# Kernel optimization log

Hardware: AMD Instinct MI355X
Metric: run time of the kernel (lower is better)

## Reference

```python
import jax, jax.numpy as jnp
import numpy as np

# ---- constants matching init_kwargs ----
NUM_CLASSES = 20
NUM_GRID = 7
NUM_BBOX = 2
IN_SIZE = 448          # image_shapes = (448, 448)
IOU_THRESHOLD = 0.7    # self.num_threshold passed to batched_nms
SCORE_THRESHOLD = 0.1  # boxes[:, -1] > 0.1 reserve mask
M = NUM_GRID * NUM_GRID  # 49 boxes per image
BATCH = 16384


def setup_inputs() -> dict:
    key = jax.random.key(0)
    out_features = M * (NUM_CLASSES + 5 * NUM_BBOX)  # 1470
    x = jax.random.uniform(key, (BATCH, out_features), dtype=jnp.float32)
    return {"x": x}


def _iou_matrix(boxes):
    # boxes: [M, 4] in (x0, y0, x1, y1). Returns [M, M] pairwise IoU.
    area = jnp.clip(boxes[:, 2] - boxes[:, 0], 0) * jnp.clip(boxes[:, 3] - boxes[:, 1], 0)
    lt = jnp.maximum(boxes[:, None, :2], boxes[None, :, :2])   # [M, M, 2]
    rb = jnp.minimum(boxes[:, None, 2:], boxes[None, :, 2:])   # [M, M, 2]
    wh = jnp.clip(rb - lt, 0)
    inter = wh[..., 0] * wh[..., 1]
    union = area[:, None] + area[None, :] - inter
    return inter / jnp.maximum(union, 1e-9)


def _nms_keep(boxes, scores, labels, valid):
    # Per-image class-aware NMS (torchvision batched_nms semantics via coordinate offsets).
    # boxes [M,4], scores [M], labels [M] int, valid [M] bool -> keep mask [M] bool.
    max_coord = jnp.max(boxes)
    offs = labels.astype(boxes.dtype) * (max_coord + 1.0)
    b = boxes + offs[:, None]
    s = jnp.where(valid, scores, -jnp.inf)
    order = jnp.argsort(-s)                 # descending by score, invalid last
    bs = b[order]
    vs = valid[order]
    iou = _iou_matrix(bs)                   # [M, M]
    idx = jnp.arange(M)

    def step(suppressed, i):
        keep_i = vs[i] & ~suppressed[i]
        suppressed = suppressed | (keep_i & (iou[i] > IOU_THRESHOLD) & (idx > i))
        return suppressed, keep_i

    _, keep_sorted = jax.lax.scan(step, jnp.zeros((M,), bool), idx)
    return jnp.zeros((M,), bool).at[order].set(keep_sorted)


def reference(x):
    N = x.shape[0]
    x = x.reshape(N, M, NUM_CLASSES + 5 * NUM_BBOX)
    class_logits = x[..., :NUM_CLASSES]                       # [N, M, C]
    bb = x[..., NUM_CLASSES:].reshape(N, M, NUM_BBOX, 5)      # [N, M, B, 5]
    # pick the bbox with max confidence per cell
    best = jnp.argmax(bb[..., 4], axis=-1)                    # [N, M]
    yolo_bboxes = jnp.take_along_axis(bb, best[..., None, None], axis=2)[:, :, 0, :]  # [N, M, 5]

    probs = jax.nn.softmax(class_logits, axis=-1)
    labels = jnp.argmax(probs, axis=-1)                       # [N, M]

    # boxes_decode: grid offsets (x tiles, y repeats) then cx/cy/w/h -> corners
    g = jnp.arange(NUM_GRID, dtype=x.dtype)
    x_grid = jnp.tile(g, NUM_GRID)                            # [M]
    y_grid = jnp.repeat(g, NUM_GRID)                          # [M]
    cx = (yolo_bboxes[..., 0] + x_grid) / NUM_GRID
    cy = (yolo_bboxes[..., 1] + y_grid) / NUM_GRID
    hw = yolo_bboxes[..., 2] / 2
    hh = yolo_bboxes[..., 3] / 2
    W = jnp.asarray(IN_SIZE, x.dtype)
    H = jnp.asarray(IN_SIZE, x.dtype)
    x0 = (cx - hw) * W
    y0 = (cy - hh) * H
    x1 = (cx + hw) * W
    y1 = (cy + hh) * H
    scores = yolo_bboxes[..., 4]
    reserve_mask = scores > SCORE_THRESHOLD                   # [N, M]

    # clip_boxes_to_image
    x0 = jnp.clip(x0, 0, IN_SIZE); x1 = jnp.clip(x1, 0, IN_SIZE)
    y0 = jnp.clip(y0, 0, IN_SIZE); y1 = jnp.clip(y1, 0, IN_SIZE)
    boxes = jnp.stack([x0, y0, x1, y1], axis=-1)              # [N, M, 4]

    keep_mask = jax.vmap(_nms_keep)(boxes, scores, labels, reserve_mask)  # [N, M]
    return class_logits, yolo_bboxes, boxes, scores, labels, keep_mask, reserve_mask
```

## Files before the change

kernel.cpp:

```cpp
#include <hip/hip_runtime.h>
#include <math.h>

#define NCLS   20
#define MCELLS 49
#define FEAT   30
#define ITEMF  1470

typedef unsigned long long u64;
typedef unsigned int u32;

__device__ __forceinline__ float bcastf(float v, int l) {
  return __int_as_float(__builtin_amdgcn_readlane(__float_as_int(v), l));
}
__device__ __forceinline__ int bcasti(int v, int l) {
  return __builtin_amdgcn_readlane(v, l);
}

__global__ __launch_bounds__(256) void yolo_post(const float* __restrict__ x,
                                                 float* __restrict__ out,
                                                 int N) {
  const int wave = threadIdx.x >> 6;
  const int lane = threadIdx.x & 63;
  const int n = blockIdx.x * 4 + wave;

  __shared__ float ldsAll[4][ITEMF];

  if (n >= N) return;

  float* L = ldsAll[wave];

  const float2* src = (const float2*)(x) + (size_t)n * (ITEMF / 2);
  float2* Ld = (float2*)L;
#pragma unroll
  for (int i = 0; i < 12; ++i) {
    int idx = lane + i * 64;
    if (idx < ITEMF / 2) Ld[idx] = src[idx];
  }
  __threadfence_block();

  const size_t NM = (size_t)N * MCELLS;
  float* out0 = out;
  float* out1 = out0 + NM * 20;
  float* out2 = out1 + NM * 5;
  float* out3 = out2 + NM * 4;
  float* out4 = out3 + NM;
  float* out5 = out4 + NM;
  float* out6 = out5 + NM;

  {
    float* dst = out0 + (size_t)n * (MCELLS * NCLS);
#pragma unroll
    for (int i = 0; i < 16; ++i) {
      int idx = lane + i * 64;
      if (idx < MCELLS * NCLS) {
        int c = idx / NCLS;
        int k = idx - c * NCLS;
        dst[idx] = L[c * FEAT + k];
      }
    }
  }

  const int m = lane;
  const bool cellv = (m < MCELLS);
  const int base = m * FEAT;

  int   labi = 0;
  float conf = 0.f;
  float x0 = 0.f, y0 = 0.f, x1 = 0.f, y1 = 0.f;
  bool reserve = false;

  if (cellv) {
    float bestv = L[base];
#pragma unroll
    for (int c = 1; c < NCLS; ++c) {
      float v = L[base + c];
      if (v > bestv) { bestv = v; labi = c; }
    }

    float c0 = L[base + 24], c1 = L[base + 29];
    int bsel = (c1 > c0) ? 1 : 0;
    int bb = base + NCLS + bsel * 5;
    float bx = L[bb], by = L[bb + 1], bw = L[bb + 2], bh = L[bb + 3];
    conf = L[bb + 4];

    float xg = (float)(m % 7), yg = (float)(m / 7);
    float cx = (bx + xg) / 7.0f, cy = (by + yg) / 7.0f;
    float hw = bw * 0.5f, hh = bh * 0.5f;
    x0 = fminf(fmaxf((cx - hw) * 448.0f, 0.f), 448.f);
    y0 = fminf(fmaxf((cy - hh) * 448.0f, 0.f), 448.f);
    x1 = fminf(fmaxf((cx + hw) * 448.0f, 0.f), 448.f);
    y1 = fminf(fmaxf((cy + hh) * 448.0f, 0.f), 448.f);
    reserve = (conf > 0.1f);

    size_t ci = (size_t)n * MCELLS + m;
    float* yb = out1 + ci * 5;
    yb[0] = bx; yb[1] = by; yb[2] = bw; yb[3] = bh; yb[4] = conf;
    *(float4*)(out2 + ci * 4) = make_float4(x0, y0, x1, y1);
    out3[ci] = conf;
    out4[ci] = (float)labi;
    out6[ci] = reserve ? 1.0f : 0.0f;
  }

  bool vld0 = cellv && reserve;
  u64 key;
  if (vld0) {
    u32 sb = __float_as_uint(conf);
    u32 inv = 0x7FFFFFFFu - sb;
    key = ((u64)labi << 37) | ((u64)inv << 6) | (u64)lane;
  } else {
    key = ~0ull;
  }

#pragma unroll
  for (int k = 2; k <= 64; k <<= 1) {
#pragma unroll
    for (int j = k >> 1; j >= 1; j >>= 1) {
      u64 ok = __shfl(key, lane ^ j);
      bool lower = (lane & j) == 0;
      bool asc = (lane & k) == 0;
      if ((key > ok) == (lower == asc)) key = ok;
    }
  }

  const int sid = (int)(key & 63);
  const bool valid = (key != ~0ull);
  const int slab = (int)((key >> 37) & 31);

  float gx0 = __shfl(x0, sid), gy0 = __shfl(y0, sid);
  float gx1 = __shfl(x1, sid), gy1 = __shfl(y1, sid);
  float garea = fmaxf(gx1 - gx0, 0.f) * fmaxf(gy1 - gy0, 0.f);

  u64 rowm = 0;
  for (int d = 1; d < MCELLS; ++d) {
    int src = (lane + d) & 63;
    int plab = __shfl(slab, src);
    bool match = (plab == slab);
    u64 anyreal = __ballot(match && (slab != 31) && (lane + d < 64));
    if (anyreal == 0) break;
    float px0 = __shfl(gx0, src), py0 = __shfl(gy0, src);
    float px1 = __shfl(gx1, src), py1 = __shfl(gy1, src);
    float pa  = bcastf(garea, 0) * 0.f + __shfl(garea, src);
    float iw = fmaxf(fminf(px1, gx1) - fmaxf(px0, gx0), 0.f);
    float ih = fmaxf(fminf(py1, gy1) - fmaxf(py0, gy0), 0.f);
    float inter = iw * ih;
    float uni = pa + garea - inter;
    bool ok = match && (inter > 0.7f * fmaxf(uni, 1e-9f));
    rowm |= ok ? (1ull << src) : 0ull;
  }

  u64 vmask = __ballot(valid);
  int V = __popcll(vmask);
  u64 supp = 0, keep = 0;
  int rlo = (int)(rowm & 0xFFFFFFFFull);
  int rhi = (int)(rowm >> 32);
  for (int i = 0; i < V; ++i) {
    if (!((supp >> i) & 1ull)) {
      keep |= 1ull << i;
      u64 rm = ((u64)(u32)bcasti(rhi, i) << 32) | (u32)bcasti(rlo, i);
      supp |= rm;
    }
  }

  int keepbit = (int)((keep >> lane) & 1ull);
  int kf = __builtin_amdgcn_ds_permute(sid << 2, __float_as_int((float)keepbit));
  if (cellv) out5[(size_t)n * MCELLS + m] = __int_as_float(kf);
}

extern "C" void kernel_launch(void* const* d_in, const int* in_sizes, int n_in,
                              void* d_out, int out_size, void* d_ws, size_t ws_size,
                              hipStream_t stream) {
  const float* x = (const float*)d_in[0];
  float* out = (float*)d_out;
  int N = in_sizes[0] / ITEMF;
  int grid = (N + 3) / 4;
  yolo_post<<<grid, 256, 0, stream>>>(x, out, N);
}
```

Before: 42.17 us.

## Process two images per wave with interleaved NMS and nontemporal stores

Each wavefront now handles two images instead of one. The sort, IoU and greedy suppression loops for both images are interleaved so their shuffle and readlane latency can overlap, which raises instruction-level parallelism. Blocks shrink to 128 threads. All output writes switch to nontemporal stores and the per-cell LDS reads use float2. The cost is more registers per lane and possibly lower occupancy, and the two images' loop trip counts are coupled, so a wave runs until the longer of the two finishes.

```diff
diff --git a/kernel.cpp b/kernel.cpp
--- a/kernel.cpp
+++ b/kernel.cpp
@@ -8,6 +8,7 @@
 
 typedef unsigned long long u64;
 typedef unsigned int u32;
+typedef float f32x4 __attribute__((ext_vector_type(4)));
 
 __device__ __forceinline__ float bcastf(float v, int l) {
   return __int_as_float(__builtin_amdgcn_readlane(__float_as_int(v), l));
@@ -15,26 +16,31 @@
 __device__ __forceinline__ int bcasti(int v, int l) {
   return __builtin_amdgcn_readlane(v, l);
 }
-
-__global__ __launch_bounds__(256) void yolo_post(const float* __restrict__ x,
+__device__ __forceinline__ void nts(float* p, float v) { __builtin_nontemporal_store(v, p); }
+
+__global__ __launch_bounds__(128) void yolo_post(const float* __restrict__ x,
                                                  float* __restrict__ out,
                                                  int N) {
   const int wave = threadIdx.x >> 6;
   const int lane = threadIdx.x & 63;
-  const int n = blockIdx.x * 4 + wave;
-
-  __shared__ float ldsAll[4][ITEMF];
-
-  if (n >= N) return;
-
-  float* L = ldsAll[wave];
-
-  const float2* src = (const float2*)(x) + (size_t)n * (ITEMF / 2);
-  float2* Ld = (float2*)L;
-#pragma unroll
-  for (int i = 0; i < 12; ++i) {
-    int idx = lane + i * 64;
-    if (idx < ITEMF / 2) Ld[idx] = src[idx];
+  const int n0 = (blockIdx.x * 2 + wave) * 2;
+
+  __shared__ float ldsAll[2][2][ITEMF];
+
+  if (n0 >= N) return;
+  const bool has1 = (n0 + 1) < N;
+  const int nn[2] = { n0, has1 ? n0 + 1 : n0 };
+  float* const LL[2] = { ldsAll[wave][0], ldsAll[wave][1] };
+
+#pragma unroll
+  for (int t = 0; t < 2; ++t) {
+    const float2* src = (const float2*)(x) + (size_t)nn[t] * (ITEMF / 2);
+    float2* Ld = (float2*)LL[t];
+#pragma unroll
+    for (int i = 0; i < 12; ++i) {
+      int idx = lane + i * 64;
+      if (idx < ITEMF / 2) Ld[idx] = src[idx];
+    }
   }
   __threadfence_block();
 
@@ -47,15 +53,18 @@
   float* out5 = out4 + NM;
   float* out6 = out5 + NM;
 
-  {
-    float* dst = out0 + (size_t)n * (MCELLS * NCLS);
+#pragma unroll
+  for (int t = 0; t < 2; ++t) {
+    if (t == 1 && !has1) break;
+    float* dst = out0 + (size_t)nn[t] * (MCELLS * NCLS);
+    const float* L = LL[t];
 #pragma unroll
     for (int i = 0; i < 16; ++i) {
       int idx = lane + i * 64;
       if (idx < MCELLS * NCLS) {
         int c = idx / NCLS;
         int k = idx - c * NCLS;
-        dst[idx] = L[c * FEAT + k];
+        nts(dst + idx, L[c * FEAT + k]);
       }
     }
   }
@@ -64,106 +73,152 @@
   const bool cellv = (m < MCELLS);
   const int base = m * FEAT;
 
-  int   labi = 0;
-  float conf = 0.f;
-  float x0 = 0.f, y0 = 0.f, x1 = 0.f, y1 = 0.f;
-  bool reserve = false;
-
-  if (cellv) {
-    float bestv = L[base];
-#pragma unroll
-    for (int c = 1; c < NCLS; ++c) {
-      float v = L[base + c];
-      if (v > bestv) { bestv = v; labi = c; }
-    }
-
-    float c0 = L[base + 24], c1 = L[base + 29];
-    int bsel = (c1 > c0) ? 1 : 0;
-    int bb = base + NCLS + bsel * 5;
-    float bx = L[bb], by = L[bb + 1], bw = L[bb + 2], bh = L[bb + 3];
-    conf = L[bb + 4];
-
-    float xg = (float)(m % 7), yg = (float)(m / 7);
-    float cx = (bx + xg) / 7.0f, cy = (by + yg) / 7.0f;
-    float hw = bw * 0.5f, hh = bh * 0.5f;
-    x0 = fminf(fmaxf((cx - hw) * 448.0f, 0.f), 448.f);
-    y0 = fminf(fmaxf((cy - hh) * 448.0f, 0.f), 448.f);
-    x1 = fminf(fmaxf((cx + hw) * 448.0f, 0.f), 448.f);
-    y1 = fminf(fmaxf((cy + hh) * 448.0f, 0.f), 448.f);
-    reserve = (conf > 0.1f);
-
-    size_t ci = (size_t)n * MCELLS + m;
-    float* yb = out1 + ci * 5;
-    yb[0] = bx; yb[1] = by; yb[2] = bw; yb[3] = bh; yb[4] = conf;
-    *(float4*)(out2 + ci * 4) = make_float4(x0, y0, x1, y1);
-    out3[ci] = conf;
-    out4[ci] = (float)labi;
-    out6[ci] = reserve ? 1.0f : 0.0f;
-  }
-
-  bool vld0 = cellv && reserve;
-  u64 key;
-  if (vld0) {
-    u32 sb = __float_as_uint(conf);
-    u32 inv = 0x7FFFFFFFu - sb;
-    key = ((u64)labi << 37) | ((u64)inv << 6) | (u64)lane;
-  } else {
-    key = ~0ull;
+  int   labi[2];
+  float conf[2];
+  float x0[2], y0[2], x1[2], y1[2];
+  bool  reserve[2];
+
+#pragma unroll
+  for (int t = 0; t < 2; ++t) {
+    labi[t] = 0; conf[t] = 0.f;
+    x0[t] = y0[t] = x1[t] = y1[t] = 0.f;
+    reserve[t] = false;
+    if (cellv) {
+      const float2* Lp = (const float2*)(LL[t] + base);
+      float bestv; int bl = 0;
+      {
+        float2 p = Lp[0];
+        bestv = p.x;
+        if (p.y > bestv) { bestv = p.y; bl = 1; }
+#pragma unroll
+        for (int j = 1; j < 10; ++j) {
+          float2 q = Lp[j];
+          if (q.x > bestv) { bestv = q.x; bl = 2 * j; }
+          if (q.y > bestv) { bestv = q.y; bl = 2 * j + 1; }
+        }
+      }
+      labi[t] = bl;
+
+      float2 q0 = Lp[10], q1 = Lp[11], q2 = Lp[12], q3 = Lp[13], q4 = Lp[14];
+      float c0 = q2.x, c1 = q4.y;
+      bool sel1 = (c1 > c0);
+      float bx = sel1 ? q2.y : q0.x;
+      float by = sel1 ? q3.x : q0.y;
+      float bw = sel1 ? q3.y : q1.x;
+      float bh = sel1 ? q4.x : q1.y;
+      float cf = sel1 ? c1 : c0;
+      conf[t] = cf;
+
+      float xg = (float)(m % 7), yg = (float)(m / 7);
+      float cx = (bx + xg) / 7.0f, cy = (by + yg) / 7.0f;
+      float hw = bw * 0.5f, hh = bh * 0.5f;
+      x0[t] = fminf(fmaxf((cx - hw) * 448.0f, 0.f), 448.f);
+      y0[t] = fminf(fmaxf((cy - hh) * 448.0f, 0.f), 448.f);
+      x1[t] = fminf(fmaxf((cx + hw) * 448.0f, 0.f), 448.f);
+      y1[t] = fminf(fmaxf((cy + hh) * 448.0f, 0.f), 448.f);
+      reserve[t] = (cf > 0.1f);
+
+      if (t == 0 || has1) {
+        size_t ci = (size_t)nn[t] * MCELLS + m;
+        float* yb = out1 + ci * 5;
+        nts(yb + 0, bx); nts(yb + 1, by); nts(yb + 2, bw); nts(yb + 3, bh); nts(yb + 4, cf);
+        f32x4 bx4 = { x0[t], y0[t], x1[t], y1[t] };
+        __builtin_nontemporal_store(bx4, (f32x4*)(out2 + ci * 4));
+        nts(out3 + ci, cf);
+        nts(out4 + ci, (float)labi[t]);
+        nts(out6 + ci, reserve[t] ? 1.0f : 0.0f);
+      }
+    }
+  }
+
+  u64 key[2];
+#pragma unroll
+  for (int t = 0; t < 2; ++t) {
+    if (cellv && reserve[t]) {
+      u32 sb = __float_as_uint(conf[t]);
+      u32 inv = 0x7FFFFFFFu - sb;
+      key[t] = ((u64)labi[t] << 37) | ((u64)inv << 6) | (u64)lane;
+    } else {
+      key[t] = ~0ull;
+    }
   }
 
 #pragma unroll
   for (int k = 2; k <= 64; k <<= 1) {
 #pragma unroll
     for (int j = k >> 1; j >= 1; j >>= 1) {
-      u64 ok = __shfl(key, lane ^ j);
+      u64 ok0 = __shfl(key[0], lane ^ j);
+      u64 ok1 = __shfl(key[1], lane ^ j);
       bool lower = (lane & j) == 0;
       bool asc = (lane & k) == 0;
-      if ((key > ok) == (lower == asc)) key = ok;
-    }
-  }
-
-  const int sid = (int)(key & 63);
-  const bool valid = (key != ~0ull);
-  const int slab = (int)((key >> 37) & 31);
-
-  float gx0 = __shfl(x0, sid), gy0 = __shfl(y0, sid);
-  float gx1 = __shfl(x1, sid), gy1 = __shfl(y1, sid);
-  float garea = fmaxf(gx1 - gx0, 0.f) * fmaxf(gy1 - gy0, 0.f);
-
-  u64 rowm = 0;
+      if ((key[0] > ok0) == (lower == asc)) key[0] = ok0;
+      if ((key[1] > ok1) == (lower == asc)) key[1] = ok1;
+    }
+  }
+
+  int  sid[2]; int slab[2];
+  float gx0[2], gy0[2], gx1[2], gy1[2], garea[2];
+#pragma unroll
+  for (int t = 0; t < 2; ++t) {
+    sid[t]  = (int)(key[t] & 63);
+    slab[t] = (int)((key[t] >> 37) & 31);
+    gx0[t] = __shfl(x0[t], sid[t]); gy0[t] = __shfl(y0[t], sid[t]);
+    gx1[t] = __shfl(x1[t], sid[t]); gy1[t] = __shfl(y1[t], sid[t]);
+    garea[t] = fmaxf(gx1[t] - gx0[t], 0.f) * fmaxf(gy1[t] - gy0[t], 0.f);
+  }
+
+  u64 rowm[2] = { 0ull, 0ull };
   for (int d = 1; d < MCELLS; ++d) {
-    int src = (lane + d) & 63;
-    int plab = __shfl(slab, src);
-    bool match = (plab == slab);
-    u64 anyreal = __ballot(match && (slab != 31) && (lane + d < 64));
-    if (anyreal == 0) break;
-    float px0 = __shfl(gx0, src), py0 = __shfl(gy0, src);
-    float px1 = __shfl(gx1, src), py1 = __shfl(gy1, src);
-    float pa  = bcastf(garea, 0) * 0.f + __shfl(garea, src);
-    float iw = fmaxf(fminf(px1, gx1) - fmaxf(px0, gx0), 0.f);
-    float ih = fmaxf(fminf(py1, gy1) - fmaxf(py0, gy0), 0.f);
-    float inter = iw * ih;
-    float uni = pa + garea - inter;
-    bool ok = match && (inter > 0.7f * fmaxf(uni, 1e-9f));
-    rowm |= ok ? (1ull << src) : 0ull;
-  }
-
-  u64 vmask = __ballot(valid);
-  int V = __popcll(vmask);
-  u64 supp = 0, keep = 0;
-  int rlo = (int)(rowm & 0xFFFFFFFFull);
-  int rhi = (int)(rowm >> 32);
-  for (int i = 0; i < V; ++i) {
-    if (!((supp >> i) & 1ull)) {
-      keep |= 1ull << i;
-      u64 rm = ((u64)(u32)bcasti(rhi, i) << 32) | (u32)bcasti(rlo, i);
-      supp |= rm;
-    }
-  }
-
-  int keepbit = (int)((keep >> lane) & 1ull);
-  int kf = __builtin_amdgcn_ds_permute(sid << 2, __float_as_int((float)keepbit));
-  if (cellv) out5[(size_t)n * MCELLS + m] = __int_as_float(kf);
+    int srcl = (lane + d) & 63;
+    bool mt[2]; u64 any[2];
+#pragma unroll
+    for (int t = 0; t < 2; ++t) {
+      int plab = __shfl(slab[t], srcl);
+      mt[t] = (plab == slab[t]) && (slab[t] != 31) && (lane + d < 64);
+      any[t] = __ballot(mt[t]);
+    }
+    if ((any[0] | any[1]) == 0ull) break;
+#pragma unroll
+    for (int t = 0; t < 2; ++t) {
+      if (any[t]) {
+        float px0 = __shfl(gx0[t], srcl), py0 = __shfl(gy0[t], srcl);
+        float px1 = __shfl(gx1[t], srcl), py1 = __shfl(gy1[t], srcl);
+        float pa  = __shfl(garea[t], srcl);
+        float iw = fmaxf(fminf(px1, gx1[t]) - fmaxf(px0, gx0[t]), 0.f);
+        float ih = fmaxf(fminf(py1, gy1[t]) - fmaxf(py0, gy0[t]), 0.f);
+        float inter = iw * ih;
+        float uni = pa + garea[t] - inter;
+        bool ok = mt[t] && (inter > 0.7f * fmaxf(uni, 1e-9f));
+        rowm[t] |= ok ? (1ull << srcl) : 0ull;
+      }
+    }
+  }
+
+  int V0 = __popcll(__ballot(key[0] != ~0ull));
+  int V1 = __popcll(__ballot(key[1] != ~0ull));
+  int rlo0 = (int)(rowm[0] & 0xFFFFFFFFull), rhi0 = (int)(rowm[0] >> 32);
+  int rlo1 = (int)(rowm[1] & 0xFFFFFFFFull), rhi1 = (int)(rowm[1] >> 32);
+  u64 supp0 = 0, keep0 = 0, supp1 = 0, keep1 = 0;
+  int Vmax = V0 > V1 ? V0 : V1;
+  for (int i = 0; i < Vmax; ++i) {
+    if (i < V0 && !((supp0 >> i) & 1ull)) {
+      keep0 |= 1ull << i;
+      supp0 |= ((u64)(u32)bcasti(rhi0, i) << 32) | (u32)bcasti(rlo0, i);
+    }
+    if (i < V1 && !((supp1 >> i) & 1ull)) {
+      keep1 |= 1ull << i;
+      supp1 |= ((u64)(u32)bcasti(rhi1, i) << 32) | (u32)bcasti(rlo1, i);
+    }
+  }
+
+  int kb0 = (int)((keep0 >> lane) & 1ull);
+  int kb1 = (int)((keep1 >> lane) & 1ull);
+  int kf0 = __builtin_amdgcn_ds_permute(sid[0] << 2, __float_as_int((float)kb0));
+  int kf1 = __builtin_amdgcn_ds_permute(sid[1] << 2, __float_as_int((float)kb1));
+  if (cellv) {
+    nts(out5 + (size_t)nn[0] * MCELLS + m, __int_as_float(kf0));
+    if (has1) nts(out5 + (size_t)nn[1] * MCELLS + m, __int_as_float(kf1));
+  }
 }
 
 extern "C" void kernel_launch(void* const* d_in, const int* in_sizes, int n_in,
@@ -172,6 +227,7 @@
   const float* x = (const float*)d_in[0];
   float* out = (float*)d_out;
   int N = in_sizes[0] / ITEMF;
-  int grid = (N + 3) / 4;
-  yolo_post<<<grid, 256, 0, stream>>>(x, out, N);
-}
+  int itemsPerBlock = 4;
+  int grid = (N + itemsPerBlock - 1) / itemsPerBlock;
+  yolo_post<<<grid, 128, 0, stream>>>(x, out, N);
+}
```

Result: slower. 55.98 us (+32.7%).
